# Kernel optimization log

Measured on AMD Instinct MI355X. Metric: run time of the kernel, lower is better.

## Reference

```python
import jax, jax.numpy as jnp
import numpy as np

B, F, E, V = 8192, 16, 32, 100000
D, H1, H2 = 8, 1024, 512
IN = F * E  # 512
EPS = 1e-5


def _bn(x, gamma, beta):
    # x: [D, B, H]; training-mode BatchNorm1d per domain over batch axis (biased var)
    mean = jnp.mean(x, axis=1, keepdims=True)
    var = jnp.mean((x - mean) ** 2, axis=1, keepdims=True)
    return (x - mean) * jax.lax.rsqrt(var + EPS) * gamma[:, None, :] + beta[:, None, :]


def setup_inputs() -> dict:
    key = jax.random.key(0)
    ks = jax.random.split(key, 12)
    feat_ids = jax.random.randint(ks[0], (B, F), 0, V)
    domain_id = jax.random.randint(ks[1], (B,), 0, D)
    emb_tables = jax.random.normal(ks[2], (F, V, E), jnp.float32) * 0.02
    s1 = 1.0 / np.sqrt(IN)
    s2 = 1.0 / np.sqrt(H1)
    s3 = 1.0 / np.sqrt(H2)
    return {
        "feat_ids": feat_ids,
        "domain_id": domain_id,
        "emb_tables": emb_tables,
        "W1": jax.random.uniform(ks[3], (D, H1, IN), jnp.float32, -s1, s1),
        "b1": jax.random.uniform(ks[4], (D, H1), jnp.float32, -s1, s1),
        "g1": jnp.ones((D, H1), jnp.float32),
        "be1": jnp.zeros((D, H1), jnp.float32),
        "W2": jax.random.uniform(ks[5], (D, H2, H1), jnp.float32, -s2, s2),
        "b2": jax.random.uniform(ks[6], (D, H2), jnp.float32, -s2, s2),
        "g2": jnp.ones((D, H2), jnp.float32),
        "be2": jnp.zeros((D, H2), jnp.float32),
        "W3": jax.random.uniform(ks[7], (D, H2), jnp.float32, -s3, s3),
        "b3": jax.random.uniform(ks[8], (D,), jnp.float32, -s3, s3),
    }


def reference(feat_ids, domain_id, emb_tables, W1, b1, g1, be1, W2, b2, g2, be2, W3, b3):
    # embedding lookup per feature then concat -> [B, F*E]
    emb = jax.vmap(lambda tab, ids: tab[ids], in_axes=(0, 1), out_axes=1)(emb_tables, feat_ids)
    emb = emb.reshape(B, IN)
    # all-domain redundant MLP (as in original torch code)
    h = jnp.einsum('bf,dhf->dbh', emb, W1) + b1[:, None, :]          # [D,B,H1]
    h = jax.nn.relu(_bn(h, g1, be1))
    h = jnp.einsum('dbh,dkh->dbk', h, W2) + b2[:, None, :]           # [D,B,H2]
    h = jax.nn.relu(_bn(h, g2, be2))
    out = jax.nn.sigmoid(jnp.einsum('dbk,dk->db', h, W3) + b3[:, None])  # [D,B]
    # mask-select the row matching each sample's domain
    final = jnp.take_along_axis(out.T, domain_id[:, None], axis=1)[:, 0]  # [B]
    return final
```

## Files before the change

### kernel.cpp

```cpp
#include <hip/hip_runtime.h>
#include <hip/hip_bf16.h>

#define B_SZ   8192
#define F_CNT  16
#define E_DIM  32
#define V_CNT  100000
#define D_CNT  8
#define H1     1024
#define H2     512
#define IN_DIM 512
#define EPS_BN 1e-5f

typedef __attribute__((ext_vector_type(8))) unsigned short ushort8;
typedef __attribute__((ext_vector_type(8))) short          frag_ab;
typedef __attribute__((ext_vector_type(4))) float          frag_cd;
typedef __attribute__((ext_vector_type(4))) float          float4v;

__device__ inline unsigned short f2b(float f) {
    unsigned int u = __builtin_bit_cast(unsigned int, f);
    unsigned int r = u + 0x7FFFu + ((u >> 16) & 1u);
    return (unsigned short)(r >> 16);
}
__device__ inline float b2f(unsigned short b) {
    return __builtin_bit_cast(float, (unsigned int)b << 16);
}

__device__ inline void ld_lds16(const unsigned short* g, unsigned short* l) {
    __builtin_amdgcn_global_load_lds(
        (const __attribute__((address_space(1))) unsigned int*)g,
        (__attribute__((address_space(3))) unsigned int*)l, 16, 0, 0);
}

__global__ void k_init(const float* __restrict__ W1, const float* __restrict__ W2,
                       const float* __restrict__ W3, const float* __restrict__ b3,
                       unsigned short* __restrict__ W1c, unsigned short* __restrict__ W2c,
                       unsigned short* __restrict__ W3c, unsigned short* __restrict__ b3c,
                       float* __restrict__ zb) {
    int bid = blockIdx.x, t = threadIdx.x;
    if (bid < 8192) {
        const float* src = (bid < 4096) ? W1 : W2;
        unsigned short* dst = (bid < 4096) ? W1c : W2c;
        long i = ((long)(bid & 4095) * 256 + t) * 4;
        float4v v = *(const float4v*)(src + i);
        dst[i]     = f2b(v[0]);
        dst[i + 1] = f2b(v[1]);
        dst[i + 2] = f2b(v[2]);
        dst[i + 3] = f2b(v[3]);
    } else if (bid == 8192) {
        const float* s = W3 + t * 16;
        unsigned short* d = W3c + t * 16;
#pragma unroll
        for (int j = 0; j < 4; j++) {
            float4v v = *(const float4v*)(s + j * 4);
            d[j * 4 + 0] = f2b(v[0]); d[j * 4 + 1] = f2b(v[1]);
            d[j * 4 + 2] = f2b(v[2]); d[j * 4 + 3] = f2b(v[3]);
        }
        if (t < D_CNT) b3c[t] = f2b(b3[t]);
    } else {
        int i = (bid - 8193) * 1024 + t * 4;
        if (i < 24576) *(float4v*)(zb + i) = (float4v){0.f, 0.f, 0.f, 0.f};
    }
}

__global__ void k_gather(const int* __restrict__ feat_ids,
                         const float* __restrict__ tables,
                         unsigned short* __restrict__ emb) {
    int tid = blockIdx.x * 256 + threadIdx.x;
    int b = tid >> 6;
    int c = tid & 63;
    int f = c >> 2;
    int id = feat_ids[b * F_CNT + f];
    const float* s = tables + ((long)f * V_CNT + id) * E_DIM + (c & 3) * 8;
    float4v v0 = *(const float4v*)s;
    float4v v1 = *(const float4v*)(s + 4);
    ushort8 o;
#pragma unroll
    for (int i = 0; i < 4; i++) { o[i] = f2b(v0[i]); o[i + 4] = f2b(v1[i]); }
    *(ushort8*)(emb + (long)b * IN_DIM + c * 8) = o;
}

__global__ __launch_bounds__(512, 2)
void k_gemm1(const unsigned short* __restrict__ A,
             const unsigned short* __restrict__ W,
             unsigned short* __restrict__ C,
             float* __restrict__ gsum, float* __restrict__ gsq,
             int M, int N, int K, long aBatchStride, int d0) {
    const int z  = blockIdx.z;
    const int m0 = blockIdx.x * 256;
    const int n0 = blockIdx.y * 256;
    const unsigned short* Ad = A + (long)z * aBatchStride;
    const unsigned short* Wd = W + (long)(d0 + z) * (long)N * K;

    __shared__ unsigned short As[2 * 2 * 8192];
    __shared__ unsigned short Bs[2 * 2 * 8192];

    const int t    = threadIdx.x;
    const int w    = t >> 6;
    const int lane = t & 63;
    const int wr   = w >> 2;
    const int wc   = w & 3;
    const int q    = lane >> 4;
    const int lr   = lane & 15;

    const int srow = lane >> 2;
    const int scol = (lane & 3) * 8;
    const unsigned short* aGb[2];
    const unsigned short* wGb[2];
    aGb[0] = Ad + (long)(m0 + w * 16 + srow) * K + scol;
    aGb[1] = aGb[0] + (long)128 * K;
    wGb[0] = Wd + (long)(n0 + w * 16 + srow) * K + scol;
    wGb[1] = wGb[0] + (long)128 * K;

    frag_cd acc[8][4];
#pragma unroll
    for (int i = 0; i < 8; i++)
#pragma unroll
        for (int j = 0; j < 4; j++)
            acc[i][j] = (frag_cd){0.f, 0.f, 0.f, 0.f};

    const int NT = K >> 6;

#pragma unroll
    for (int p = 0; p < 4; ++p) {
        const int kh = p >> 1, sg = p & 1;
        ld_lds16(aGb[sg] + kh * 32, &As[kh * 8192 + sg * 4096 + w * 512]);
        ld_lds16(wGb[sg] + kh * 32, &Bs[kh * 8192 + sg * 4096 + w * 512]);
    }

    for (int tt = 0; tt < NT; ++tt) {
        const int b = tt & 1;
        const bool lastT = (tt == NT - 1);
#pragma unroll
        for (int p = 0; p < 4; ++p) {
            const int ks = p >> 1;
            const int mh = p & 1;
            if (p == 0 || p == 2) {
                if (p == 2 && lastT)
                    asm volatile("s_waitcnt vmcnt(0)" ::: "memory");
                else
                    asm volatile("s_waitcnt vmcnt(4)" ::: "memory");
                __builtin_amdgcn_s_barrier();
            }
            frag_ab af[4], bf[4];
            const unsigned short* Ap = &As[b * 16384 + ks * 8192];
            const unsigned short* Bp = &Bs[b * 16384 + ks * 8192];
#pragma unroll
            for (int i = 0; i < 4; ++i) {
                af[i] = *(const frag_ab*)&Ap[(wr * 128 + (mh * 4 + i) * 16 + lr) * 32 + q * 8];
                bf[i] = *(const frag_ab*)&Bp[(wc * 64 + i * 16 + lr) * 32 + q * 8];
            }
            if (!lastT) {
                const long ko = (long)(tt + 1) * 64 + ks * 32;
                ld_lds16(aGb[mh] + ko, &As[(b ^ 1) * 16384 + ks * 8192 + mh * 4096 + w * 512]);
                ld_lds16(wGb[mh] + ko, &Bs[(b ^ 1) * 16384 + ks * 8192 + mh * 4096 + w * 512]);
            }
            __builtin_amdgcn_s_barrier();
            asm volatile("s_waitcnt lgkmcnt(0)" ::: "memory");
            __builtin_amdgcn_sched_barrier(0);
            __builtin_amdgcn_s_setprio(1);
#pragma unroll
            for (int i = 0; i < 4; ++i)
#pragma unroll
                for (int j = 0; j < 4; ++j)
                    acc[mh * 4 + i][j] = __builtin_amdgcn_mfma_f32_16x16x32_bf16(
                        af[i], bf[j], acc[mh * 4 + i][j], 0, 0, 0);
            __builtin_amdgcn_s_setprio(0);
            __builtin_amdgcn_s_barrier();
        }
    }

    unsigned short* Cd = C + (long)z * (long)M * N;
    float s[4], q2[4];
#pragma unroll
    for (int j = 0; j < 4; j++) { s[j] = 0.f; q2[j] = 0.f; }
#pragma unroll
    for (int I = 0; I < 8; ++I) {
        int row = m0 + wr * 128 + I * 16 + q * 4;
#pragma unroll
        for (int j = 0; j < 4; ++j) {
            int col = n0 + wc * 64 + j * 16 + lr;
#pragma unroll
            for (int r = 0; r < 4; ++r) {
                float v = acc[I][j][r];
                Cd[(long)(row + r) * N + col] = f2b(v);
                s[j] += v; q2[j] += v * v;
            }
        }
    }
#pragma unroll
    for (int j = 0; j < 4; j++) {
        s[j]  += __shfl_xor(s[j], 16, 64);  s[j]  += __shfl_xor(s[j], 32, 64);
        q2[j] += __shfl_xor(q2[j], 16, 64); q2[j] += __shfl_xor(q2[j], 32, 64);
    }
    if (lane < 16) {
        float* gs = gsum + (long)(d0 + z) * N + n0 + wc * 64;
        float* gq = gsq  + (long)(d0 + z) * N + n0 + wc * 64;
#pragma unroll
        for (int j = 0; j < 4; j++) {
            atomicAdd(&gs[j * 16 + lane], s[j]);
            atomicAdd(&gq[j * 16 + lane], q2[j]);
        }
    }
}

__device__ inline void gemm_epilogue(frag_cd acc[4][4],
                                     unsigned short* __restrict__ Cd,
                                     float* __restrict__ gsum, float* __restrict__ gsq,
                                     int N, int d, int m0, int n0,
                                     int wm, int wn, int q, int lr, int lane) {
    float s[4], q2[4];
#pragma unroll
    for (int j = 0; j < 4; j++) { s[j] = 0.f; q2[j] = 0.f; }
#pragma unroll
    for (int i = 0; i < 4; i++) {
        int row = m0 + wm + i * 16 + q * 4;
#pragma unroll
        for (int j = 0; j < 4; j++) {
            int col = n0 + wn + j * 16 + lr;
#pragma unroll
            for (int r = 0; r < 4; r++) {
                float v = acc[i][j][r];
                Cd[(long)(row + r) * N + col] = f2b(v);
                s[j] += v; q2[j] += v * v;
            }
        }
    }
#pragma unroll
    for (int j = 0; j < 4; j++) {
        s[j]  += __shfl_xor(s[j], 16, 64);  s[j]  += __shfl_xor(s[j], 32, 64);
        q2[j] += __shfl_xor(q2[j], 16, 64); q2[j] += __shfl_xor(q2[j], 32, 64);
    }
    if (lane < 16) {
        float* gs = gsum + (long)d * N + n0 + wn;
        float* gq = gsq  + (long)d * N + n0 + wn;
#pragma unroll
        for (int j = 0; j < 4; j++) {
            atomicAdd(&gs[j * 16 + lane], s[j]);
            atomicAdd(&gq[j * 16 + lane], q2[j]);
        }
    }
}

__global__ __launch_bounds__(256, 2)
void k_gemm2(const unsigned short* __restrict__ A,
             const unsigned short* __restrict__ W,
             unsigned short* __restrict__ C,
             float* __restrict__ gsum, float* __restrict__ gsq,
             const float* __restrict__ sc1, const float* __restrict__ sh1,
             int M, int N, int K, long aBatchStride, int d0) {
    const int z  = blockIdx.z;
    const int m0 = blockIdx.x * 128;
    const int n0 = blockIdx.y * 128;
    const unsigned short* Ad = A + (long)z * aBatchStride;
    const unsigned short* Wd = W + (long)(d0 + z) * N * K;

    __shared__ unsigned short As[128 * 32];
    __shared__ unsigned short Bs[128 * 32];

    const int t    = threadIdx.x;
    const int wave = t >> 6;
    const int lane = t & 63;
    const int wm   = (wave & 1) << 6;
    const int wn   = (wave >> 1) << 6;
    const int q    = lane >> 4;
    const int lr   = lane & 15;

    const int srow = lane >> 2;
    const int scol = (lane & 3) * 8;
    const unsigned short* aP0 = Ad + (long)(m0 + wave * 32 + srow) * K + scol;
    const unsigned short* aP1 = aP0 + 16 * (long)K;
    const float* scD = sc1 + (long)(d0 + z) * K;
    const float* shD = sh1 + (long)(d0 + z) * K;
    const unsigned short* wG0 = Wd + (long)(n0 + wave * 32 + srow) * K + scol;
    const unsigned short* wG1 = wG0 + 16 * (long)K;
    unsigned short* aL0w = &As[(wave * 32 + srow) * 32 + scol];
    unsigned short* aL1w = aL0w + 16 * 32;
    unsigned short* wL0 = &Bs[(wave * 32) * 32];
    unsigned short* wL1 = &Bs[(wave * 32 + 16) * 32];

    frag_cd acc[4][4];
#pragma unroll
    for (int i = 0; i < 4; i++)
#pragma unroll
        for (int j = 0; j < 4; j++)
            acc[i][j] = (frag_cd){0.f, 0.f, 0.f, 0.f};

    ushort8 x0 = *(const ushort8*)aP0;
    ushort8 x1 = *(const ushort8*)aP1;

    for (int k0 = 0; k0 < K; k0 += 32) {
        ld_lds16(wG0 + k0, wL0);
        ld_lds16(wG1 + k0, wL1);
        float4v sa = *(const float4v*)(scD + k0 + scol);
        float4v sb = *(const float4v*)(scD + k0 + scol + 4);
        float4v ha = *(const float4v*)(shD + k0 + scol);
        float4v hb = *(const float4v*)(shD + k0 + scol + 4);
        ushort8 y0, y1;
#pragma unroll
        for (int i2 = 0; i2 < 8; i2++) {
            float scv = (i2 < 4) ? sa[i2] : sb[i2 - 4];
            float shv = (i2 < 4) ? ha[i2] : hb[i2 - 4];
            y0[i2] = f2b(fmaxf(b2f(x0[i2]) * scv + shv, 0.f));
            y1[i2] = f2b(fmaxf(b2f(x1[i2]) * scv + shv, 0.f));
        }
        *(ushort8*)aL0w = y0;
        *(ushort8*)aL1w = y1;
        __syncthreads();

        if (k0 + 32 < K) {
            x0 = *(const ushort8*)(aP0 + k0 + 32);
            x1 = *(const ushort8*)(aP1 + k0 + 32);
        }

        frag_ab af[4], bf[4];
#pragma unroll
        for (int i = 0; i < 4; i++) {
            af[i] = *(const frag_ab*)&As[(wm + i * 16 + lr) * 32 + q * 8];
            bf[i] = *(const frag_ab*)&Bs[(wn + i * 16 + lr) * 32 + q * 8];
        }
#pragma unroll
        for (int i = 0; i < 4; i++)
#pragma unroll
            for (int j = 0; j < 4; j++)
                acc[i][j] = __builtin_amdgcn_mfma_f32_16x16x32_bf16(af[i], bf[j], acc[i][j], 0, 0, 0);
        __syncthreads();
    }

    unsigned short* Cd = C + (long)z * M * N;
    gemm_epilogue(acc, Cd, gsum, gsq, N, d0 + z, m0, n0, wm, wn, q, lr, lane);
}

__global__ void k_finalize(const float* __restrict__ gsum, const float* __restrict__ gsq,
                           const float* __restrict__ g, const float* __restrict__ be,
                           float* __restrict__ scale, float* __restrict__ shift, int n,
                           int gOff) {
    int i = blockIdx.x * 256 + threadIdx.x;
    if (i >= n) return;
    float mean = gsum[i] * (1.0f / B_SZ);
    float var  = gsq[i] * (1.0f / B_SZ) - mean * mean;
    float sc   = g[gOff + i] * rsqrtf(var + EPS_BN);
    scale[i] = sc;
    shift[i] = be[gOff + i] - mean * sc;
}

__global__ void k_final(const unsigned short* __restrict__ h2c,
                        const int* __restrict__ domain_id,
                        const float* __restrict__ scale2, const float* __restrict__ shift2,
                        const unsigned short* __restrict__ W3, const unsigned short* __restrict__ b3,
                        float* __restrict__ out, int d0, int nc) {
    int wave = threadIdx.x >> 6, lane = threadIdx.x & 63;
    int b = blockIdx.x * 4 + wave;
    int d = domain_id[b];
    if (d < d0 || d >= d0 + nc) return;
    int o = d * H2 + lane * 8;
    ushort8 v = *(const ushort8*)(h2c + ((long)(d - d0) * B_SZ + b) * H2 + lane * 8);
    ushort8 w = *(const ushort8*)(W3 + o);
    float sum = 0.f;
#pragma unroll
    for (int i = 0; i < 8; i++) {
        float x = b2f(v[i]) * scale2[o + i] + shift2[o + i];
        sum += fmaxf(x, 0.f) * b2f(w[i]);
    }
#pragma unroll
    for (int off = 32; off > 0; off >>= 1) sum += __shfl_xor(sum, off, 64);
    if (lane == 0)
        out[b] = 1.f / (1.f + expf(-(sum + b2f(b3[d]))));
}

__global__ void k_sentinel(float* __restrict__ out, int n) {
    int i = blockIdx.x * 256 + threadIdx.x;
    if (i < n) out[i] = 0.25f;
}

extern "C" void kernel_launch(void* const* d_in, const int* in_sizes, int n_in,
                              void* d_out, int out_size, void* d_ws, size_t ws_size,
                              hipStream_t stream) {
    const int*   feat_ids  = (const int*)d_in[0];
    const int*   domain_id = (const int*)d_in[1];
    const float* tables = (const float*)d_in[2];
    const float* W1  = (const float*)d_in[3];
    const float* g1  = (const float*)d_in[5];
    const float* be1 = (const float*)d_in[6];
    const float* W2  = (const float*)d_in[7];
    const float* g2  = (const float*)d_in[9];
    const float* be2 = (const float*)d_in[10];
    const float* W3  = (const float*)d_in[11];
    const float* b3  = (const float*)d_in[12];

    char* ws = (char*)d_ws;
    float* gsum1  = (float*)ws;
    float* gsq1   = gsum1 + 8192;
    float* gsum2  = gsq1 + 8192;
    float* gsq2   = gsum2 + 4096;
    float* scale1 = gsq2 + 4096;
    float* shift1 = scale1 + 8192;
    float* scale2 = shift1 + 8192;
    float* shift2 = scale2 + 4096;
    unsigned short* W1c = (unsigned short*)(ws + (1L  << 20));
    unsigned short* W2c = (unsigned short*)(ws + (9L  << 20));
    unsigned short* W3c = (unsigned short*)(ws + (17L << 20));
    unsigned short* b3c = W3c + D_CNT * H2;
    unsigned short* emb = (unsigned short*)(ws + (18L << 20));

    const long h1Elems = (long)B_SZ * H1;
    const long h2Elems = (long)B_SZ * H2;
    const long perDom  = (h1Elems + h2Elems) * 2;
    const long baseOff = 26L << 20;
    int NC = 0;
    for (int cand = 8; cand >= 1; cand >>= 1)
        if (baseOff + (long)cand * perDom <= (long)ws_size) { NC = cand; break; }
    if (NC == 0) {
        k_sentinel<<<dim3((out_size + 255) / 256), dim3(256), 0, stream>>>(
            (float*)d_out, out_size);
        return;
    }
    unsigned short* h1c = (unsigned short*)(ws + baseOff);
    unsigned short* h2c = h1c + (long)NC * h1Elems;

    k_init<<<dim3(8217), dim3(256), 0, stream>>>(W1, W2, W3, b3, W1c, W2c, W3c, b3c, gsum1);
    k_gather<<<dim3(2048), dim3(256), 0, stream>>>(feat_ids, tables, emb);

    for (int d0 = 0; d0 < D_CNT; d0 += NC) {
        k_gemm1<<<dim3(32, 4, NC), dim3(512), 0, stream>>>(
            emb, W1c, h1c, gsum1, gsq1, 8192, 1024, 512, 0L, d0);
        k_finalize<<<dim3(NC * 4), dim3(256), 0, stream>>>(
            gsum1 + d0 * H1, gsq1 + d0 * H1, g1, be1,
            scale1 + d0 * H1, shift1 + d0 * H1, NC * H1, d0 * H1);
        k_gemm2<<<dim3(64, 4, NC), dim3(256), 0, stream>>>(
            h1c, W2c, h2c, gsum2, gsq2, scale1, shift1, 8192, 512, 1024, h1Elems, d0);
        k_finalize<<<dim3(NC * 2), dim3(256), 0, stream>>>(
            gsum2 + d0 * H2, gsq2 + d0 * H2, g2, be2,
            scale2 + d0 * H2, shift2 + d0 * H2, NC * H2, d0 * H2);
        k_final<<<dim3(2048), dim3(256), 0, stream>>>(
            h2c, domain_id, scale2, shift2, W3c, b3c, (float*)d_out, d0, NC);
    }
}
```

Baseline: 478.5 us.

## Rewrite gemm2 as 256x256 double-buffered tile and store only matching-domain rows

k_gemm2 moves from a 128x128 tile with 256 threads and one sync per k-step to a 256x256 tile with 512 threads. It double-buffers LDS and software-pipelines the BN1+ReLU transform of the A operand one step ahead. BN scale and shift are staged in LDS, and the epilogue writes h2 only for rows whose domain_id matches, since the final kernel reads only those rows. k_gemm1's inner loop is also restructured to do all 8 M sub-tiles per k-half with fewer barriers. The aim is more operand reuse, fewer barriers and less store traffic, at the cost of more register pressure and a more fragile waitcnt schedule.

```diff
diff --git a/kernel.cpp b/kernel.cpp
--- a/kernel.cpp
+++ b/kernel.cpp
@@ -15,6 +15,7 @@
 typedef __attribute__((ext_vector_type(8))) short          frag_ab;
 typedef __attribute__((ext_vector_type(4))) float          frag_cd;
 typedef __attribute__((ext_vector_type(4))) float          float4v;
+typedef __attribute__((ext_vector_type(2))) float          float2v;
 
 __device__ inline unsigned short f2b(float f) {
     unsigned int u = __builtin_bit_cast(unsigned int, f);
@@ -101,15 +102,13 @@
     const int wc   = w & 3;
     const int q    = lane >> 4;
     const int lr   = lane & 15;
-
     const int srow = lane >> 2;
     const int scol = (lane & 3) * 8;
-    const unsigned short* aGb[2];
-    const unsigned short* wGb[2];
-    aGb[0] = Ad + (long)(m0 + w * 16 + srow) * K + scol;
-    aGb[1] = aGb[0] + (long)128 * K;
-    wGb[0] = Wd + (long)(n0 + w * 16 + srow) * K + scol;
-    wGb[1] = wGb[0] + (long)128 * K;
+
+    const unsigned short* aG0 = Ad + (long)(m0 + w * 16 + srow) * K + scol;
+    const unsigned short* aG1 = aG0 + 128 * (long)K;
+    const unsigned short* wG0 = Wd + (long)(n0 + w * 16 + srow) * K + scol;
+    const unsigned short* wG1 = wG0 + 128 * (long)K;
 
     frag_cd acc[8][4];
 #pragma unroll
@@ -121,51 +120,48 @@
     const int NT = K >> 6;
 
 #pragma unroll
-    for (int p = 0; p < 4; ++p) {
-        const int kh = p >> 1, sg = p & 1;
-        ld_lds16(aGb[sg] + kh * 32, &As[kh * 8192 + sg * 4096 + w * 512]);
-        ld_lds16(wGb[sg] + kh * 32, &Bs[kh * 8192 + sg * 4096 + w * 512]);
+    for (int ks = 0; ks < 2; ++ks) {
+        ld_lds16(aG0 + ks * 32, &As[ks * 8192 + w * 512]);
+        ld_lds16(aG1 + ks * 32, &As[ks * 8192 + 4096 + w * 512]);
+        ld_lds16(wG0 + ks * 32, &Bs[ks * 8192 + w * 512]);
+        ld_lds16(wG1 + ks * 32, &Bs[ks * 8192 + 4096 + w * 512]);
     }
 
     for (int tt = 0; tt < NT; ++tt) {
         const int b = tt & 1;
         const bool lastT = (tt == NT - 1);
 #pragma unroll
-        for (int p = 0; p < 4; ++p) {
-            const int ks = p >> 1;
-            const int mh = p & 1;
-            if (p == 0 || p == 2) {
-                if (p == 2 && lastT)
-                    asm volatile("s_waitcnt vmcnt(0)" ::: "memory");
-                else
-                    asm volatile("s_waitcnt vmcnt(4)" ::: "memory");
-                __builtin_amdgcn_s_barrier();
+        for (int ks = 0; ks < 2; ++ks) {
+            if (lastT && ks == 1)
+                asm volatile("s_waitcnt vmcnt(0)" ::: "memory");
+            else
+                asm volatile("s_waitcnt vmcnt(4)" ::: "memory");
+            __builtin_amdgcn_s_barrier();
+            if (!lastT) {
+                const long ko = (long)(tt + 1) * 64 + ks * 32;
+                const int  db = (b ^ 1) * 16384 + ks * 8192 + w * 512;
+                ld_lds16(aG0 + ko, &As[db]);
+                ld_lds16(aG1 + ko, &As[db + 4096]);
+                ld_lds16(wG0 + ko, &Bs[db]);
+                ld_lds16(wG1 + ko, &Bs[db + 4096]);
             }
-            frag_ab af[4], bf[4];
+            frag_ab af[8], bf[4];
             const unsigned short* Ap = &As[b * 16384 + ks * 8192];
             const unsigned short* Bp = &Bs[b * 16384 + ks * 8192];
 #pragma unroll
-            for (int i = 0; i < 4; ++i) {
-                af[i] = *(const frag_ab*)&Ap[(wr * 128 + (mh * 4 + i) * 16 + lr) * 32 + q * 8];
-                bf[i] = *(const frag_ab*)&Bp[(wc * 64 + i * 16 + lr) * 32 + q * 8];
-            }
-            if (!lastT) {
-                const long ko = (long)(tt + 1) * 64 + ks * 32;
-                ld_lds16(aGb[mh] + ko, &As[(b ^ 1) * 16384 + ks * 8192 + mh * 4096 + w * 512]);
-                ld_lds16(wGb[mh] + ko, &Bs[(b ^ 1) * 16384 + ks * 8192 + mh * 4096 + w * 512]);
-            }
-            __builtin_amdgcn_s_barrier();
-            asm volatile("s_waitcnt lgkmcnt(0)" ::: "memory");
-            __builtin_amdgcn_sched_barrier(0);
+            for (int i = 0; i < 8; ++i)
+                af[i] = *(const frag_ab*)&Ap[(wr * 128 + i * 16 + lr) * 32 + q * 8];
+#pragma unroll
+            for (int j = 0; j < 4; ++j)
+                bf[j] = *(const frag_ab*)&Bp[(wc * 64 + j * 16 + lr) * 32 + q * 8];
             __builtin_amdgcn_s_setprio(1);
 #pragma unroll
-            for (int i = 0; i < 4; ++i)
+            for (int i = 0; i < 8; ++i)
 #pragma unroll
                 for (int j = 0; j < 4; ++j)
-                    acc[mh * 4 + i][j] = __builtin_amdgcn_mfma_f32_16x16x32_bf16(
-                        af[i], bf[j], acc[mh * 4 + i][j], 0, 0, 0);
+                    acc[i][j] = __builtin_amdgcn_mfma_f32_16x16x32_bf16(
+                        af[i], bf[j], acc[i][j], 0, 0, 0);
             __builtin_amdgcn_s_setprio(0);
-            __builtin_amdgcn_s_barrier();
         }
     }
 
@@ -203,98 +199,73 @@
     }
 }
 
-__device__ inline void gemm_epilogue(frag_cd acc[4][4],
-                                     unsigned short* __restrict__ Cd,
-                                     float* __restrict__ gsum, float* __restrict__ gsq,
-                                     int N, int d, int m0, int n0,
-                                     int wm, int wn, int q, int lr, int lane) {
-    float s[4], q2[4];
-#pragma unroll
-    for (int j = 0; j < 4; j++) { s[j] = 0.f; q2[j] = 0.f; }
-#pragma unroll
-    for (int i = 0; i < 4; i++) {
-        int row = m0 + wm + i * 16 + q * 4;
-#pragma unroll
-        for (int j = 0; j < 4; j++) {
-            int col = n0 + wn + j * 16 + lr;
-#pragma unroll
-            for (int r = 0; r < 4; r++) {
-                float v = acc[i][j][r];
-                Cd[(long)(row + r) * N + col] = f2b(v);
-                s[j] += v; q2[j] += v * v;
-            }
-        }
-    }
-#pragma unroll
-    for (int j = 0; j < 4; j++) {
-        s[j]  += __shfl_xor(s[j], 16, 64);  s[j]  += __shfl_xor(s[j], 32, 64);
-        q2[j] += __shfl_xor(q2[j], 16, 64); q2[j] += __shfl_xor(q2[j], 32, 64);
-    }
-    if (lane < 16) {
-        float* gs = gsum + (long)d * N + n0 + wn;
-        float* gq = gsq  + (long)d * N + n0 + wn;
-#pragma unroll
-        for (int j = 0; j < 4; j++) {
-            atomicAdd(&gs[j * 16 + lane], s[j]);
-            atomicAdd(&gq[j * 16 + lane], q2[j]);
-        }
-    }
-}
-
-__global__ __launch_bounds__(256, 2)
+__global__ __launch_bounds__(512, 2)
 void k_gemm2(const unsigned short* __restrict__ A,
              const unsigned short* __restrict__ W,
              unsigned short* __restrict__ C,
              float* __restrict__ gsum, float* __restrict__ gsq,
              const float* __restrict__ sc1, const float* __restrict__ sh1,
+             const int* __restrict__ dom,
              int M, int N, int K, long aBatchStride, int d0) {
-    const int z  = blockIdx.z;
-    const int m0 = blockIdx.x * 128;
-    const int n0 = blockIdx.y * 128;
+    const int z    = blockIdx.z;
+    const int m0   = blockIdx.x * 256;
+    const int n0   = blockIdx.y * 256;
+    const int dcur = d0 + z;
     const unsigned short* Ad = A + (long)z * aBatchStride;
-    const unsigned short* Wd = W + (long)(d0 + z) * N * K;
-
-    __shared__ unsigned short As[128 * 32];
-    __shared__ unsigned short Bs[128 * 32];
+    const unsigned short* Wd = W + (long)dcur * (long)N * K;
+
+    __shared__ unsigned short As[2 * 2 * 8192];
+    __shared__ unsigned short Bs[2 * 2 * 8192];
+    __shared__ float scLds[1024];
+    __shared__ float shLds[1024];
 
     const int t    = threadIdx.x;
-    const int wave = t >> 6;
+    const int w    = t >> 6;
     const int lane = t & 63;
-    const int wm   = (wave & 1) << 6;
-    const int wn   = (wave >> 1) << 6;
+    const int wr   = w >> 2;
+    const int wc   = w & 3;
     const int q    = lane >> 4;
     const int lr   = lane & 15;
-
     const int srow = lane >> 2;
     const int scol = (lane & 3) * 8;
-    const unsigned short* aP0 = Ad + (long)(m0 + wave * 32 + srow) * K + scol;
-    const unsigned short* aP1 = aP0 + 16 * (long)K;
-    const float* scD = sc1 + (long)(d0 + z) * K;
-    const float* shD = sh1 + (long)(d0 + z) * K;
-    const unsigned short* wG0 = Wd + (long)(n0 + wave * 32 + srow) * K + scol;
-    const unsigned short* wG1 = wG0 + 16 * (long)K;
-    unsigned short* aL0w = &As[(wave * 32 + srow) * 32 + scol];
-    unsigned short* aL1w = aL0w + 16 * 32;
-    unsigned short* wL0 = &Bs[(wave * 32) * 32];
-    unsigned short* wL1 = &Bs[(wave * 32 + 16) * 32];
-
-    frag_cd acc[4][4];
-#pragma unroll
-    for (int i = 0; i < 4; i++)
+
+    const unsigned short* aG0 = Ad + (long)(m0 + w * 16 + srow) * K + scol;
+    const unsigned short* aG1 = aG0 + 128 * (long)K;
+    const unsigned short* wG0 = Wd + (long)(n0 + w * 16 + srow) * K + scol;
+    const unsigned short* wG1 = wG0 + 128 * (long)K;
+    const float* scD = sc1 + (long)dcur * K;
+    const float* shD = sh1 + (long)dcur * K;
+
+    frag_cd acc[8][4];
+#pragma unroll
+    for (int i = 0; i < 8; i++)
 #pragma unroll
         for (int j = 0; j < 4; j++)
             acc[i][j] = (frag_cd){0.f, 0.f, 0.f, 0.f};
 
-    ushort8 x0 = *(const ushort8*)aP0;
-    ushort8 x1 = *(const ushort8*)aP1;
-
-    for (int k0 = 0; k0 < K; k0 += 32) {
-        ld_lds16(wG0 + k0, wL0);
-        ld_lds16(wG1 + k0, wL1);
-        float4v sa = *(const float4v*)(scD + k0 + scol);
-        float4v sb = *(const float4v*)(scD + k0 + scol + 4);
-        float4v ha = *(const float4v*)(shD + k0 + scol);
-        float4v hb = *(const float4v*)(shD + k0 + scol + 4);
+    const int NT = K >> 6;
+
+    ld_lds16(wG0,      &Bs[w * 512]);
+    ld_lds16(wG1,      &Bs[4096 + w * 512]);
+    ld_lds16(wG0 + 32, &Bs[8192 + w * 512]);
+    ld_lds16(wG1 + 32, &Bs[8192 + 4096 + w * 512]);
+    ushort8 p00 = *(const ushort8*)aG0;
+    ushort8 p01 = *(const ushort8*)aG1;
+    ushort8 p10 = *(const ushort8*)(aG0 + 32);
+    ushort8 p11 = *(const ushort8*)(aG1 + 32);
+    *(float2v*)&scLds[t * 2] = *(const float2v*)&scD[t * 2];
+    *(float2v*)&shLds[t * 2] = *(const float2v*)&shD[t * 2];
+    __syncthreads();
+
+#pragma unroll
+    for (int ks = 0; ks < 2; ++ks) {
+        const int kp = ks * 32 + scol;
+        float4v sa = *(const float4v*)&scLds[kp];
+        float4v sb = *(const float4v*)&scLds[kp + 4];
+        float4v ha = *(const float4v*)&shLds[kp];
+        float4v hb = *(const float4v*)&shLds[kp + 4];
+        ushort8 x0 = ks ? p10 : p00;
+        ushort8 x1 = ks ? p11 : p01;
         ushort8 y0, y1;
 #pragma unroll
         for (int i2 = 0; i2 < 8; i2++) {
@@ -303,31 +274,116 @@
             y0[i2] = f2b(fmaxf(b2f(x0[i2]) * scv + shv, 0.f));
             y1[i2] = f2b(fmaxf(b2f(x1[i2]) * scv + shv, 0.f));
         }
-        *(ushort8*)aL0w = y0;
-        *(ushort8*)aL1w = y1;
-        __syncthreads();
-
-        if (k0 + 32 < K) {
-            x0 = *(const ushort8*)(aP0 + k0 + 32);
-            x1 = *(const ushort8*)(aP1 + k0 + 32);
-        }
-
-        frag_ab af[4], bf[4];
-#pragma unroll
-        for (int i = 0; i < 4; i++) {
-            af[i] = *(const frag_ab*)&As[(wm + i * 16 + lr) * 32 + q * 8];
-            bf[i] = *(const frag_ab*)&Bs[(wn + i * 16 + lr) * 32 + q * 8];
-        }
-#pragma unroll
-        for (int i = 0; i < 4; i++)
-#pragma unroll
-            for (int j = 0; j < 4; j++)
-                acc[i][j] = __builtin_amdgcn_mfma_f32_16x16x32_bf16(af[i], bf[j], acc[i][j], 0, 0, 0);
-        __syncthreads();
-    }
-
-    unsigned short* Cd = C + (long)z * M * N;
-    gemm_epilogue(acc, Cd, gsum, gsq, N, d0 + z, m0, n0, wm, wn, q, lr, lane);
+        *(ushort8*)&As[ks * 8192 + w * 512 + lane * 8] = y0;
+        *(ushort8*)&As[ks * 8192 + 4096 + w * 512 + lane * 8] = y1;
+    }
+    __syncthreads();
+
+    ushort8 xp0, xp1;
+    int pOff = 0;
+
+    for (int tt = 0; tt < NT; ++tt) {
+        const int b = tt & 1;
+        const bool lastT = (tt == NT - 1);
+#pragma unroll
+        for (int ks = 0; ks < 2; ++ks) {
+            if (lastT && ks == 1)
+                asm volatile("s_waitcnt vmcnt(0)" ::: "memory");
+            else
+                asm volatile("s_waitcnt vmcnt(4)" ::: "memory");
+            __builtin_amdgcn_s_barrier();
+
+            ushort8 xn0, xn1; int nOff;
+            if (!lastT) {
+                const long ko = (long)(tt + 1) * 64 + ks * 32;
+                const int  db = ((tt + 1) & 1) * 16384 + ks * 8192 + w * 512;
+                ld_lds16(wG0 + ko, &Bs[db]);
+                ld_lds16(wG1 + ko, &Bs[db + 4096]);
+                xn0 = *(const ushort8*)(aG0 + ko);
+                xn1 = *(const ushort8*)(aG1 + ko);
+                nOff = db;
+            } else { xn0 = xp0; xn1 = xp1; nOff = pOff; }
+
+            const bool pend = ks ? (tt < NT - 1) : (tt > 0);
+            if (pend) {
+                if (!lastT) asm volatile("s_waitcnt vmcnt(4)" ::: "memory");
+                else        asm volatile("s_waitcnt vmcnt(0)" ::: "memory");
+                const int kp = tt * 64 + 32 + ks * 32 + scol;
+                float4v sa = *(const float4v*)&scLds[kp];
+                float4v sb = *(const float4v*)&scLds[kp + 4];
+                float4v ha = *(const float4v*)&shLds[kp];
+                float4v hb = *(const float4v*)&shLds[kp + 4];
+                ushort8 y0, y1;
+#pragma unroll
+                for (int i2 = 0; i2 < 8; i2++) {
+                    float scv = (i2 < 4) ? sa[i2] : sb[i2 - 4];
+                    float shv = (i2 < 4) ? ha[i2] : hb[i2 - 4];
+                    y0[i2] = f2b(fmaxf(b2f(xp0[i2]) * scv + shv, 0.f));
+                    y1[i2] = f2b(fmaxf(b2f(xp1[i2]) * scv + shv, 0.f));
+                }
+                *(ushort8*)&As[pOff + lane * 8] = y0;
+                *(ushort8*)&As[pOff + 4096 + lane * 8] = y1;
+            }
+            xp0 = xn0; xp1 = xn1; pOff = nOff;
+
+            frag_ab af[8], bf[4];
+            const unsigned short* Ap = &As[b * 16384 + ks * 8192];
+            const unsigned short* Bp = &Bs[b * 16384 + ks * 8192];
+#pragma unroll
+            for (int i = 0; i < 8; ++i)
+                af[i] = *(const frag_ab*)&Ap[(wr * 128 + i * 16 + lr) * 32 + q * 8];
+#pragma unroll
+            for (int j = 0; j < 4; ++j)
+                bf[j] = *(const frag_ab*)&Bp[(wc * 64 + j * 16 + lr) * 32 + q * 8];
+            asm volatile("s_waitcnt lgkmcnt(0)" ::: "memory");
+            __builtin_amdgcn_sched_barrier(0);
+            __builtin_amdgcn_s_setprio(1);
+#pragma unroll
+            for (int i = 0; i < 8; ++i)
+#pragma unroll
+                for (int j = 0; j < 4; ++j)
+                    acc[i][j] = __builtin_amdgcn_mfma_f32_16x16x32_bf16(
+                        af[i], bf[j], acc[i][j], 0, 0, 0);
+            __builtin_amdgcn_s_setprio(0);
+        }
+    }
+
+    unsigned short* Cd = C + (long)z * (long)M * N;
+    float s[4], q2[4];
+#pragma unroll
+    for (int j = 0; j < 4; j++) { s[j] = 0.f; q2[j] = 0.f; }
+#pragma unroll
+    for (int I = 0; I < 8; ++I) {
+        int row = m0 + wr * 128 + I * 16 + q * 4;
+        int dm[4];
+#pragma unroll
+        for (int r = 0; r < 4; ++r) dm[r] = dom[row + r];
+#pragma unroll
+        for (int j = 0; j < 4; ++j) {
+            int col = n0 + wc * 64 + j * 16 + lr;
+#pragma unroll
+            for (int r = 0; r < 4; ++r) {
+                float v = acc[I][j][r];
+                s[j] += v; q2[j] += v * v;
+                if (dm[r] == dcur)
+                    Cd[(long)(row + r) * N + col] = f2b(v);
+            }
+        }
+    }
+#pragma unroll
+    for (int j = 0; j < 4; j++) {
+        s[j]  += __shfl_xor(s[j], 16, 64);  s[j]  += __shfl_xor(s[j], 32, 64);
+        q2[j] += __shfl_xor(q2[j], 16, 64); q2[j] += __shfl_xor(q2[j], 32, 64);
+    }
+    if (lane < 16) {
+        float* gs = gsum + (long)dcur * N + n0 + wc * 64;
+        float* gq = gsq  + (long)dcur * N + n0 + wc * 64;
+#pragma unroll
+        for (int j = 0; j < 4; j++) {
+            atomicAdd(&gs[j * 16 + lane], s[j]);
+            atomicAdd(&gq[j * 16 + lane], q2[j]);
+        }
+    }
 }
 
 __global__ void k_finalize(const float* __restrict__ gsum, const float* __restrict__ gsq,
@@ -426,8 +482,9 @@
         k_finalize<<<dim3(NC * 4), dim3(256), 0, stream>>>(
             gsum1 + d0 * H1, gsq1 + d0 * H1, g1, be1,
             scale1 + d0 * H1, shift1 + d0 * H1, NC * H1, d0 * H1);
-        k_gemm2<<<dim3(64, 4, NC), dim3(256), 0, stream>>>(
-            h1c, W2c, h2c, gsum2, gsq2, scale1, shift1, 8192, 512, 1024, h1Elems, d0);
+        k_gemm2<<<dim3(32, 2, NC), dim3(512), 0, stream>>>(
+            h1c, W2c, h2c, gsum2, gsq2, scale1, shift1, domain_id,
+            8192, 512, 1024, h1Elems, d0);
         k_finalize<<<dim3(NC * 2), dim3(256), 0, stream>>>(
             gsum2 + d0 * H2, gsq2 + d0 * H2, g2, be2,
             scale2 + d0 * H2, shift2 + d0 * H2, NC * H2, d0 * H2);
```

Result: slower. 508.6 us (+6.3%).

## Widen gemm2 tile to full N=512 so BN1+ReLU on A runs once per row

Applied to the files above, without the earlier changes.

The second GEMM now uses 512-thread blocks that each cover 128 rows by all 512 output columns, with 8 waves each computing a 64x128 sub-tile. Previously four column blocks each reloaded and re-normalized the same A rows, so the fused BN1 scale/shift/ReLU and the A reads were repeated four times. Now they happen once per row. The cost is a larger LDS footprint for B, 128 accumulator registers per lane, and a grid a quarter the size, which may hurt occupancy and latency hiding.

```diff
diff --git a/kernel.cpp b/kernel.cpp
--- a/kernel.cpp
+++ b/kernel.cpp
@@ -203,131 +203,121 @@
     }
 }
 
-__device__ inline void gemm_epilogue(frag_cd acc[4][4],
-                                     unsigned short* __restrict__ Cd,
-                                     float* __restrict__ gsum, float* __restrict__ gsq,
-                                     int N, int d, int m0, int n0,
-                                     int wm, int wn, int q, int lr, int lane) {
-    float s[4], q2[4];
-#pragma unroll
-    for (int j = 0; j < 4; j++) { s[j] = 0.f; q2[j] = 0.f; }
-#pragma unroll
-    for (int i = 0; i < 4; i++) {
-        int row = m0 + wm + i * 16 + q * 4;
-#pragma unroll
-        for (int j = 0; j < 4; j++) {
-            int col = n0 + wn + j * 16 + lr;
-#pragma unroll
-            for (int r = 0; r < 4; r++) {
-                float v = acc[i][j][r];
-                Cd[(long)(row + r) * N + col] = f2b(v);
-                s[j] += v; q2[j] += v * v;
-            }
-        }
-    }
-#pragma unroll
-    for (int j = 0; j < 4; j++) {
-        s[j]  += __shfl_xor(s[j], 16, 64);  s[j]  += __shfl_xor(s[j], 32, 64);
-        q2[j] += __shfl_xor(q2[j], 16, 64); q2[j] += __shfl_xor(q2[j], 32, 64);
-    }
-    if (lane < 16) {
-        float* gs = gsum + (long)d * N + n0 + wn;
-        float* gq = gsq  + (long)d * N + n0 + wn;
-#pragma unroll
-        for (int j = 0; j < 4; j++) {
-            atomicAdd(&gs[j * 16 + lane], s[j]);
-            atomicAdd(&gq[j * 16 + lane], q2[j]);
-        }
-    }
-}
-
-__global__ __launch_bounds__(256, 2)
+__global__ __launch_bounds__(512, 2)
 void k_gemm2(const unsigned short* __restrict__ A,
              const unsigned short* __restrict__ W,
              unsigned short* __restrict__ C,
              float* __restrict__ gsum, float* __restrict__ gsq,
              const float* __restrict__ sc1, const float* __restrict__ sh1,
              int M, int N, int K, long aBatchStride, int d0) {
-    const int z  = blockIdx.z;
-    const int m0 = blockIdx.x * 128;
-    const int n0 = blockIdx.y * 128;
+    const int z    = blockIdx.z;
+    const int m0   = blockIdx.x * 128;
+    const int dcur = d0 + z;
     const unsigned short* Ad = A + (long)z * aBatchStride;
-    const unsigned short* Wd = W + (long)(d0 + z) * N * K;
+    const unsigned short* Wd = W + (long)dcur * (long)N * K;
 
     __shared__ unsigned short As[128 * 32];
-    __shared__ unsigned short Bs[128 * 32];
+    __shared__ unsigned short Bs[512 * 32];
 
     const int t    = threadIdx.x;
-    const int wave = t >> 6;
+    const int w    = t >> 6;
     const int lane = t & 63;
-    const int wm   = (wave & 1) << 6;
-    const int wn   = (wave >> 1) << 6;
+    const int wm   = (w & 1) << 6;
+    const int wn   = (w >> 1) << 7;
     const int q    = lane >> 4;
     const int lr   = lane & 15;
-
     const int srow = lane >> 2;
     const int scol = (lane & 3) * 8;
-    const unsigned short* aP0 = Ad + (long)(m0 + wave * 32 + srow) * K + scol;
-    const unsigned short* aP1 = aP0 + 16 * (long)K;
-    const float* scD = sc1 + (long)(d0 + z) * K;
-    const float* shD = sh1 + (long)(d0 + z) * K;
-    const unsigned short* wG0 = Wd + (long)(n0 + wave * 32 + srow) * K + scol;
-    const unsigned short* wG1 = wG0 + 16 * (long)K;
-    unsigned short* aL0w = &As[(wave * 32 + srow) * 32 + scol];
-    unsigned short* aL1w = aL0w + 16 * 32;
-    unsigned short* wL0 = &Bs[(wave * 32) * 32];
-    unsigned short* wL1 = &Bs[(wave * 32 + 16) * 32];
-
-    frag_cd acc[4][4];
+
+    const unsigned short* aP = Ad + (long)(m0 + w * 16 + srow) * K + scol;
+    unsigned short* aLw = &As[(w * 16 + srow) * 32 + scol];
+    const float* scD = sc1 + (long)dcur * K;
+    const float* shD = sh1 + (long)dcur * K;
+    const unsigned short* wG[4];
+    unsigned short* wL[4];
+#pragma unroll
+    for (int i = 0; i < 4; ++i) {
+        wG[i] = Wd + (long)(w * 64 + i * 16 + srow) * K + scol;
+        wL[i] = &Bs[(w * 64 + i * 16) * 32];
+    }
+
+    frag_cd acc[4][8];
 #pragma unroll
     for (int i = 0; i < 4; i++)
 #pragma unroll
-        for (int j = 0; j < 4; j++)
+        for (int j = 0; j < 8; j++)
             acc[i][j] = (frag_cd){0.f, 0.f, 0.f, 0.f};
 
-    ushort8 x0 = *(const ushort8*)aP0;
-    ushort8 x1 = *(const ushort8*)aP1;
+    ushort8 x0 = *(const ushort8*)aP;
 
     for (int k0 = 0; k0 < K; k0 += 32) {
-        ld_lds16(wG0 + k0, wL0);
-        ld_lds16(wG1 + k0, wL1);
+#pragma unroll
+        for (int i = 0; i < 4; ++i)
+            ld_lds16(wG[i] + k0, wL[i]);
         float4v sa = *(const float4v*)(scD + k0 + scol);
         float4v sb = *(const float4v*)(scD + k0 + scol + 4);
         float4v ha = *(const float4v*)(shD + k0 + scol);
         float4v hb = *(const float4v*)(shD + k0 + scol + 4);
-        ushort8 y0, y1;
+        ushort8 y0;
 #pragma unroll
         for (int i2 = 0; i2 < 8; i2++) {
             float scv = (i2 < 4) ? sa[i2] : sb[i2 - 4];
             float shv = (i2 < 4) ? ha[i2] : hb[i2 - 4];
             y0[i2] = f2b(fmaxf(b2f(x0[i2]) * scv + shv, 0.f));
-            y1[i2] = f2b(fmaxf(b2f(x1[i2]) * scv + shv, 0.f));
-        }
-        *(ushort8*)aL0w = y0;
-        *(ushort8*)aL1w = y1;
+        }
+        *(ushort8*)aLw = y0;
         __syncthreads();
 
-        if (k0 + 32 < K) {
-            x0 = *(const ushort8*)(aP0 + k0 + 32);
-            x1 = *(const ushort8*)(aP1 + k0 + 32);
-        }
-
-        frag_ab af[4], bf[4];
-#pragma unroll
-        for (int i = 0; i < 4; i++) {
+        if (k0 + 32 < K)
+            x0 = *(const ushort8*)(aP + k0 + 32);
+
+        frag_ab af[4], bf[8];
+#pragma unroll
+        for (int i = 0; i < 4; i++)
             af[i] = *(const frag_ab*)&As[(wm + i * 16 + lr) * 32 + q * 8];
-            bf[i] = *(const frag_ab*)&Bs[(wn + i * 16 + lr) * 32 + q * 8];
-        }
+#pragma unroll
+        for (int j = 0; j < 8; j++)
+            bf[j] = *(const frag_ab*)&Bs[(wn + j * 16 + lr) * 32 + q * 8];
 #pragma unroll
         for (int i = 0; i < 4; i++)
 #pragma unroll
-            for (int j = 0; j < 4; j++)
+            for (int j = 0; j < 8; j++)
                 acc[i][j] = __builtin_amdgcn_mfma_f32_16x16x32_bf16(af[i], bf[j], acc[i][j], 0, 0, 0);
         __syncthreads();
     }
 
-    unsigned short* Cd = C + (long)z * M * N;
-    gemm_epilogue(acc, Cd, gsum, gsq, N, d0 + z, m0, n0, wm, wn, q, lr, lane);
+    unsigned short* Cd = C + (long)z * (long)M * N;
+    float s[8], q2[8];
+#pragma unroll
+    for (int j = 0; j < 8; j++) { s[j] = 0.f; q2[j] = 0.f; }
+#pragma unroll
+    for (int i = 0; i < 4; i++) {
+        int row = m0 + wm + i * 16 + q * 4;
+#pragma unroll
+        for (int j = 0; j < 8; j++) {
+            int col = wn + j * 16 + lr;
+#pragma unroll
+            for (int r = 0; r < 4; r++) {
+                float v = acc[i][j][r];
+                Cd[(long)(row + r) * N + col] = f2b(v);
+                s[j] += v; q2[j] += v * v;
+            }
+        }
+    }
+#pragma unroll
+    for (int j = 0; j < 8; j++) {
+        s[j]  += __shfl_xor(s[j], 16, 64);  s[j]  += __shfl_xor(s[j], 32, 64);
+        q2[j] += __shfl_xor(q2[j], 16, 64); q2[j] += __shfl_xor(q2[j], 32, 64);
+    }
+    if (lane < 16) {
+        float* gs = gsum + (long)dcur * N + wn;
+        float* gq = gsq  + (long)dcur * N + wn;
+#pragma unroll
+        for (int j = 0; j < 8; j++) {
+            atomicAdd(&gs[j * 16 + lane], s[j]);
+            atomicAdd(&gq[j * 16 + lane], q2[j]);
+        }
+    }
 }
 
 __global__ void k_finalize(const float* __restrict__ gsum, const float* __restrict__ gsq,
@@ -426,7 +416,7 @@
         k_finalize<<<dim3(NC * 4), dim3(256), 0, stream>>>(
             gsum1 + d0 * H1, gsq1 + d0 * H1, g1, be1,
             scale1 + d0 * H1, shift1 + d0 * H1, NC * H1, d0 * H1);
-        k_gemm2<<<dim3(64, 4, NC), dim3(256), 0, stream>>>(
+        k_gemm2<<<dim3(64, 1, NC), dim3(512), 0, stream>>>(
             h1c, W2c, h2c, gsum2, gsq2, scale1, shift1, 8192, 512, 1024, h1Elems, d0);
         k_finalize<<<dim3(NC * 2), dim3(256), 0, stream>>>(
             gsum2 + d0 * H2, gsq2 + d0 * H2, g2, be2,
```

Result: no change. 479.9 us (+0.3%).
